# Performance work log

Measured on AMD Instinct MI355X. Metric: run time of the kernel, lower is better.

Reference implementation:

```python
import jax, jax.numpy as jnp
import numpy as np

N_NODES = 50000
N_EDGES = 1600000
N_GRAPHS = 64
D = 128


def setup_inputs() -> dict:
    key = jax.random.key(0)
    ks = jax.random.split(key, 6)
    x = jax.random.normal(ks[0], (N_NODES, D), dtype=jnp.float32)
    W1 = jax.random.normal(ks[1], (D, D), dtype=jnp.float32) * (1.0 / np.sqrt(D))
    b1 = jnp.zeros((D,), dtype=jnp.float32)
    W2 = jax.random.normal(ks[2], (D, D), dtype=jnp.float32) * (1.0 / np.sqrt(D))
    b2 = jnp.zeros((D,), dtype=jnp.float32)
    edge_index = jax.random.randint(ks[3], (2, N_EDGES), 0, N_NODES, dtype=jnp.int64)
    batch = jnp.sort(jax.random.randint(ks[4], (N_NODES,), 0, N_GRAPHS, dtype=jnp.int64))
    return {"x": x, "W1": W1, "b1": b1, "W2": W2, "b2": b2,
            "edge_index": edge_index, "batch": batch}


def _gcn_conv(x, W, b, src, dst, coef, n_nodes):
    # GCNConv: h = W^T x; out_i = sum_{j->i} norm_ij * h_j + b
    h = x @ W                                  # [N, D_out]
    msg = h[src] * coef[:, None]               # [E+N, D_out] gather + scale
    out = jax.ops.segment_sum(msg, dst, num_segments=n_nodes)
    return out + b


def reference(x, W1, b1, W2, b2, edge_index, batch):
    n_nodes = x.shape[0]
    # add self-loops (PyG GCNConv default add_self_loops=True)
    loop = jnp.arange(n_nodes, dtype=edge_index.dtype)
    src = jnp.concatenate([edge_index[0], loop])
    dst = jnp.concatenate([edge_index[1], loop])
    # symmetric normalization: deg counted on target side incl. self-loops
    deg = jax.ops.segment_sum(jnp.ones_like(dst, dtype=x.dtype), dst,
                              num_segments=n_nodes)
    dinv = jnp.where(deg > 0, jax.lax.rsqrt(deg), 0.0)
    coef = dinv[src] * dinv[dst]               # [E+N]

    h = jax.nn.relu(_gcn_conv(x, W1, b1, src, dst, coef, n_nodes))
    h = jax.nn.relu(_gcn_conv(h, W2, b2, src, dst, coef, n_nodes))

    # global_mean_pool over batch ids
    sums = jax.ops.segment_sum(h, batch, num_segments=N_GRAPHS)
    cnts = jax.ops.segment_sum(jnp.ones((n_nodes,), dtype=h.dtype), batch,
                               num_segments=N_GRAPHS)
    return sums / jnp.maximum(cnts, 1.0)[:, None]
```

## Files before the change

### kernel.cpp

```cpp
#include <hip/hip_runtime.h>
#include <stdint.h>

#define DF 128
#define PAD 80
#define BCAP 8192
#define PCHUNK 16

typedef __attribute__((ext_vector_type(8))) __bf16 bf16x8;
typedef __attribute__((ext_vector_type(4))) float f32x4;

__device__ inline unsigned bf16rn(float x) {
    unsigned u = __float_as_uint(x);
    return (u + 0x7FFFu + ((u >> 16) & 1u)) >> 16;
}
__device__ inline float4 unpack_bf16x4(uint2 v) {
    float4 r;
    r.x = __uint_as_float(v.x << 16);
    r.y = __uint_as_float(v.x & 0xFFFF0000u);
    r.z = __uint_as_float(v.y << 16);
    r.w = __uint_as_float(v.y & 0xFFFF0000u);
    return r;
}

__global__ __launch_bounds__(256) void bucket_kernel(const int* __restrict__ src,
        const int* __restrict__ dst, int* __restrict__ gcursor,
        unsigned* __restrict__ buckets, int E) {
    __shared__ int hist[256];
    __shared__ int base[256];
    __shared__ int loc[256];
    int tid = threadIdx.x;
    hist[tid] = 0; loc[tid] = 0;
    __syncthreads();
    int beg = blockIdx.x * BCAP;
    int end = beg + BCAP; if (end > E) end = E;
    for (int i = beg + tid; i < end; i += 256) {
        int d = dst[i];
        atomicAdd(&hist[d >> 8], 1);
    }
    __syncthreads();
    base[tid] = atomicAdd(&gcursor[tid], hist[tid]);
    __syncthreads();
    for (int i = beg + tid; i < end; i += 256) {
        int d = dst[i];
        int s = __builtin_nontemporal_load(src + i);
        int b = d >> 8;
        int r = atomicAdd(&loc[b], 1);
        int pos = base[b] + r;
        if (pos < BCAP)
            buckets[(size_t)b * BCAP + pos] = ((unsigned)(d & 255) << 16) | (unsigned)s;
    }
}

__global__ __launch_bounds__(256) void csr_kernel(const unsigned* __restrict__ buckets,
        const int* __restrict__ gcursor, unsigned short* __restrict__ csr,
        int* __restrict__ cnt, float* __restrict__ dinv, int N) {
    __shared__ int nodecnt[256];
    int tid = threadIdx.x;
    nodecnt[tid] = 0;
    __syncthreads();
    int b = blockIdx.x;
    int nb = gcursor[b]; if (nb > BCAP) nb = BCAP;
    const unsigned* __restrict__ bk = buckets + (size_t)b * BCAP;
    for (int i = tid; i < nb; i += 256) {
        unsigned w = bk[i];
        int dl = w >> 16;
        int r = atomicAdd(&nodecnt[dl], 1);
        if (r < PAD)
            csr[(size_t)(b * 256 + dl) * PAD + r] = (unsigned short)(w & 0xFFFFu);
    }
    __syncthreads();
    int node = b * 256 + tid;
    if (node < N) {
        int c = nodecnt[tid];
        cnt[node] = c;
        dinv[node] = rsqrtf((float)(c + 1));
    }
}

__global__ void bounds_kernel(const int* __restrict__ batch, int* __restrict__ gse, int n, int G) {
    int i = blockIdx.x * blockDim.x + threadIdx.x;
    if (i < n) {
        int b = batch[i];
        if (i == 0 || batch[i - 1] != b) gse[b] = i;
        if (i == n - 1 || batch[i + 1] != b) gse[G + b] = i + 1;
    }
}

__global__ __launch_bounds__(256) void gemm_mfma(
    const float* __restrict__ A, const float* __restrict__ W,
    const float* __restrict__ dinv, uint2* __restrict__ g2, int N)
{
    __shared__ unsigned short Wt[128 * 136];
    int tid = threadIdx.x;
    int wv = tid >> 6;
    int l  = tid & 63;
    int lr = l & 15;
    int lk = (l >> 4) * 8;
    int r  = blockIdx.x * 64 + wv * 16 + lr;
    int rc = (r < N) ? r : (N - 1);

    float4 areg[8];
    const float* Arow = A + (size_t)rc * DF;
    #pragma unroll
    for (int ks = 0; ks < 4; ++ks) {
        areg[2 * ks]     = *(const float4*)(Arow + ks * 32 + lk);
        areg[2 * ks + 1] = *(const float4*)(Arow + ks * 32 + lk + 4);
    }

    #pragma unroll
    for (int i = 0; i < 16; ++i) {
        int flat = i * 256 + tid;
        int k = flat >> 5;
        int c4 = (flat & 31) << 2;
        float4 w4 = *(const float4*)(W + (size_t)k * DF + c4);
        Wt[(c4 + 0) * 136 + k] = (unsigned short)bf16rn(w4.x);
        Wt[(c4 + 1) * 136 + k] = (unsigned short)bf16rn(w4.y);
        Wt[(c4 + 2) * 136 + k] = (unsigned short)bf16rn(w4.z);
        Wt[(c4 + 3) * 136 + k] = (unsigned short)bf16rn(w4.w);
    }

    union U8 { unsigned short s[8]; bf16x8 v; };
    bf16x8 aH[4], aL[4];
    #pragma unroll
    for (int ks = 0; ks < 4; ++ks) {
        U8 uh, ul;
        const float* f0 = (const float*)&areg[2 * ks];
        #pragma unroll
        for (int j = 0; j < 8; ++j) {
            float a = f0[j];
            unsigned hb = bf16rn(a);
            float hf = __uint_as_float(hb << 16);
            uh.s[j] = (unsigned short)hb;
            ul.s[j] = (unsigned short)bf16rn(a - hf);
        }
        aH[ks] = uh.v; aL[ks] = ul.v;
    }

    __syncthreads();

    f32x4 zero = {0.f, 0.f, 0.f, 0.f};
    f32x4 acc[8];
    #pragma unroll
    for (int t = 0; t < 8; ++t) acc[t] = zero;

    #pragma unroll
    for (int ks = 0; ks < 4; ++ks) {
        int ko = ks * 32 + lk;
        #pragma unroll
        for (int t = 0; t < 8; ++t) {
            bf16x8 wf = *(const bf16x8*)&Wt[(t * 16 + lr) * 136 + ko];
            acc[t] = __builtin_amdgcn_mfma_f32_16x16x32_bf16(wf, aH[ks], acc[t], 0, 0, 0);
            acc[t] = __builtin_amdgcn_mfma_f32_16x16x32_bf16(wf, aL[ks], acc[t], 0, 0, 0);
        }
    }

    if (r < N) {
        float di = dinv[r];
        int hi4 = l >> 4;
        #pragma unroll
        for (int t = 0; t < 8; ++t) {
            unsigned lo = bf16rn(di * acc[t][0]) | (bf16rn(di * acc[t][1]) << 16);
            unsigned hi = bf16rn(di * acc[t][2]) | (bf16rn(di * acc[t][3]) << 16);
            uint2 o; o.x = lo; o.y = hi;
            g2[(size_t)r * 32 + t * 4 + hi4] = o;
        }
    }
}

__global__ __launch_bounds__(256) void agg_kernel(
    const uint2* __restrict__ g, const unsigned short* __restrict__ csr,
    const int* __restrict__ cnt, const float* __restrict__ dinv,
    const float* __restrict__ bias, float* __restrict__ out, int n)
{
    int idx = blockIdx.x * 256 + threadIdx.x;
    int node = idx >> 5;
    int lane = threadIdx.x & 31;
    if (node >= n) return;
    int deg = cnt[node]; if (deg > PAD) deg = PAD;
    const unsigned short* __restrict__ row = csr + (size_t)node * PAD;

    float4 a0 = unpack_bf16x4(g[(size_t)node * 32 + lane]);
    float4 a1 = {0.f, 0.f, 0.f, 0.f};
    float4 a2 = {0.f, 0.f, 0.f, 0.f};
    float4 a3 = {0.f, 0.f, 0.f, 0.f};

    int e = 0;
    for (; e + 7 < deg; e += 8) {
        uint4 w = *(const uint4*)(row + e);
        int s0 = (int)(w.x & 0xFFFFu), s1 = (int)(w.x >> 16);
        int s2 = (int)(w.y & 0xFFFFu), s3 = (int)(w.y >> 16);
        int s4 = (int)(w.z & 0xFFFFu), s5 = (int)(w.z >> 16);
        int s6 = (int)(w.w & 0xFFFFu), s7 = (int)(w.w >> 16);
        uint2 v0 = g[(size_t)s0 * 32 + lane];
        uint2 v1 = g[(size_t)s1 * 32 + lane];
        uint2 v2 = g[(size_t)s2 * 32 + lane];
        uint2 v3 = g[(size_t)s3 * 32 + lane];
        uint2 v4 = g[(size_t)s4 * 32 + lane];
        uint2 v5 = g[(size_t)s5 * 32 + lane];
        uint2 v6 = g[(size_t)s6 * 32 + lane];
        uint2 v7 = g[(size_t)s7 * 32 + lane];
        float4 f0 = unpack_bf16x4(v0), f1 = unpack_bf16x4(v1);
        float4 f2 = unpack_bf16x4(v2), f3 = unpack_bf16x4(v3);
        float4 f4 = unpack_bf16x4(v4), f5 = unpack_bf16x4(v5);
        float4 f6 = unpack_bf16x4(v6), f7 = unpack_bf16x4(v7);
        a0.x += f0.x + f4.x; a0.y += f0.y + f4.y; a0.z += f0.z + f4.z; a0.w += f0.w + f4.w;
        a1.x += f1.x + f5.x; a1.y += f1.y + f5.y; a1.z += f1.z + f5.z; a1.w += f1.w + f5.w;
        a2.x += f2.x + f6.x; a2.y += f2.y + f6.y; a2.z += f2.z + f6.z; a2.w += f2.w + f6.w;
        a3.x += f3.x + f7.x; a3.y += f3.y + f7.y; a3.z += f3.z + f7.z; a3.w += f3.w + f7.w;
    }
    for (; e + 3 < deg; e += 4) {
        int s0 = row[e], s1 = row[e + 1], s2 = row[e + 2], s3 = row[e + 3];
        uint2 v0 = g[(size_t)s0 * 32 + lane];
        uint2 v1 = g[(size_t)s1 * 32 + lane];
        uint2 v2 = g[(size_t)s2 * 32 + lane];
        uint2 v3 = g[(size_t)s3 * 32 + lane];
        float4 f0 = unpack_bf16x4(v0), f1 = unpack_bf16x4(v1);
        float4 f2 = unpack_bf16x4(v2), f3 = unpack_bf16x4(v3);
        a0.x += f0.x; a0.y += f0.y; a0.z += f0.z; a0.w += f0.w;
        a1.x += f1.x; a1.y += f1.y; a1.z += f1.z; a1.w += f1.w;
        a2.x += f2.x; a2.y += f2.y; a2.z += f2.z; a2.w += f2.w;
        a3.x += f3.x; a3.y += f3.y; a3.z += f3.z; a3.w += f3.w;
    }
    for (; e < deg; ++e) {
        uint2 v = g[(size_t)row[e] * 32 + lane];
        float4 f = unpack_bf16x4(v);
        a0.x += f.x; a0.y += f.y; a0.z += f.z; a0.w += f.w;
    }
    float sx = (a0.x + a1.x) + (a2.x + a3.x);
    float sy = (a0.y + a1.y) + (a2.y + a3.y);
    float sz = (a0.z + a1.z) + (a2.z + a3.z);
    float sw = (a0.w + a1.w) + (a2.w + a3.w);

    float di = dinv[node];
    float4 b4 = ((const float4*)bias)[lane];
    float4 o;
    o.x = fmaxf(fmaf(di, sx, b4.x), 0.f);
    o.y = fmaxf(fmaf(di, sy, b4.y), 0.f);
    o.z = fmaxf(fmaf(di, sz, b4.z), 0.f);
    o.w = fmaxf(fmaf(di, sw, b4.w), 0.f);
    ((float4*)out)[(size_t)node * 32 + lane] = o;
}

__global__ __launch_bounds__(256) void pool_partial(
    const float* __restrict__ h, const int* __restrict__ gse,
    float* __restrict__ acc, int G)
{
    __shared__ float part[256];
    int gi = blockIdx.x >> 4;
    int ck = blockIdx.x & (PCHUNK - 1);
    int s = gse[gi], e = gse[G + gi];
    int len = e - s;
    if (len <= 0) return;
    int per = (len + PCHUNK - 1) / PCHUNK;
    int r0 = s + ck * per;
    int r1 = r0 + per; if (r1 > e) r1 = e;
    int c = threadIdx.x & 127;
    int rr = threadIdx.x >> 7;
    float sum = 0.f;
    for (int r = r0 + rr; r < r1; r += 2) sum += h[(size_t)r * DF + c];
    part[threadIdx.x] = sum;
    __syncthreads();
    if (threadIdx.x < 128) {
        float t = part[threadIdx.x] + part[threadIdx.x + 128];
        atomicAdd(&acc[gi * DF + c], t);
    }
}

__global__ __launch_bounds__(128) void pool_final(
    const float* __restrict__ acc, const int* __restrict__ gse,
    float* __restrict__ out, int G)
{
    int gi = blockIdx.x;
    int c = threadIdx.x;
    int s = gse[gi], e = gse[G + gi];
    out[gi * DF + c] = (e > s) ? (acc[gi * DF + c] / (float)(e - s)) : 0.f;
}

extern "C" void kernel_launch(void* const* d_in, const int* in_sizes, int n_in,
                              void* d_out, int out_size, void* d_ws, size_t ws_size,
                              hipStream_t stream)
{
    const float* x     = (const float*)d_in[0];
    const float* W1    = (const float*)d_in[1];
    const float* b1    = (const float*)d_in[2];
    const float* W2    = (const float*)d_in[3];
    const float* b2    = (const float*)d_in[4];
    const int*   ei    = (const int*)d_in[5];
    const int*   batch = (const int*)d_in[6];

    int N = in_sizes[0] / DF;
    int E = in_sizes[5] / 2;
    int G = out_size / DF;
    const int* src = ei;
    const int* dst = ei + E;

    int nbuck = (N + 255) >> 8;

    char* p = (char*)d_ws;
    int* gcursor = (int*)p; p += (size_t)256 * 4;
    int* gse     = (int*)p; p += (size_t)2 * G * 4;
    float* acc   = (float*)p; p += (size_t)G * DF * 4;
    int* cnt     = (int*)p; p += (size_t)N * 4;
    float* dinv  = (float*)p; p += (size_t)N * 4;
    unsigned* buckets = (unsigned*)p; p += (size_t)nbuck * BCAP * 4;
    unsigned short* csr = (unsigned short*)p; p += (size_t)N * PAD * 2;
    p = (char*)(((uintptr_t)p + 15) & ~(uintptr_t)15);
    uint2* g2 = (uint2*)p; p += (size_t)N * DF * 2;
    float* h  = (float*)p; p += (size_t)N * DF * 4;

    hipMemsetAsync(gcursor, 0, (size_t)(256 + 2 * G + G * DF) * 4, stream);

    const int thr = 256;
    int nb1 = (E + BCAP - 1) / BCAP;

    bounds_kernel<<<(N + thr - 1) / thr, thr, 0, stream>>>(batch, gse, N, G);
    bucket_kernel<<<nb1, thr, 0, stream>>>(src, dst, gcursor, buckets, E);
    csr_kernel<<<nbuck, thr, 0, stream>>>(buckets, gcursor, csr, cnt, dinv, N);

    int gemm_grid = (N + 63) / 64;
    int agg_grid  = (N * 32 + 255) / 256;

    gemm_mfma<<<gemm_grid, thr, 0, stream>>>(x, W1, dinv, g2, N);
    agg_kernel<<<agg_grid, thr, 0, stream>>>(g2, csr, cnt, dinv, b1, h, N);
    gemm_mfma<<<gemm_grid, thr, 0, stream>>>(h, W2, dinv, g2, N);
    agg_kernel<<<agg_grid, thr, 0, stream>>>(g2, csr, cnt, dinv, b2, h, N);
    pool_partial<<<G * PCHUNK, thr, 0, stream>>>(h, gse, acc, G);
    pool_final<<<G, 128, 0, stream>>>(acc, gse, (float*)d_out, G);
}
```

Before: 216.6 us.

## Fuse mean-pool partial sums into second aggregation and merge bounds into CSR build

The second aggregation kernel now stages each block's 8 output rows in shared memory and accumulates per-graph column sums with atomics, replacing the separate pool_partial kernel that re-read h. The graph-boundary computation moves into csr_kernel, which removes one launch. The gather loop is unrolled to 16 neighbours per iteration to keep more loads in flight. The cost is more atomics (one set per block) plus a __syncthreads and shared memory in the aggregation kernel; the output h is still written even though the pooled path no longer needs it.

Result: no change. 220.1 us (+1.6%).

```diff
diff --git a/kernel.cpp b/kernel.cpp
--- a/kernel.cpp
+++ b/kernel.cpp
@@ -4,7 +4,6 @@
 #define DF 128
 #define PAD 80
 #define BCAP 8192
-#define PCHUNK 16
 
 typedef __attribute__((ext_vector_type(8))) __bf16 bf16x8;
 typedef __attribute__((ext_vector_type(4))) float f32x4;
@@ -20,6 +19,9 @@
     r.z = __uint_as_float(v.y << 16);
     r.w = __uint_as_float(v.y & 0xFFFF0000u);
     return r;
+}
+__device__ inline void addf4(float4& a, float4 f) {
+    a.x += f.x; a.y += f.y; a.z += f.z; a.w += f.w;
 }
 
 __global__ __launch_bounds__(256) void bucket_kernel(const int* __restrict__ src,
@@ -53,7 +55,8 @@
 
 __global__ __launch_bounds__(256) void csr_kernel(const unsigned* __restrict__ buckets,
         const int* __restrict__ gcursor, unsigned short* __restrict__ csr,
-        int* __restrict__ cnt, float* __restrict__ dinv, int N) {
+        int* __restrict__ cnt, float* __restrict__ dinv,
+        const int* __restrict__ batch, int* __restrict__ gse, int N, int G) {
     __shared__ int nodecnt[256];
     int tid = threadIdx.x;
     nodecnt[tid] = 0;
@@ -74,15 +77,9 @@
         int c = nodecnt[tid];
         cnt[node] = c;
         dinv[node] = rsqrtf((float)(c + 1));
-    }
-}
-
-__global__ void bounds_kernel(const int* __restrict__ batch, int* __restrict__ gse, int n, int G) {
-    int i = blockIdx.x * blockDim.x + threadIdx.x;
-    if (i < n) {
-        int b = batch[i];
-        if (i == 0 || batch[i - 1] != b) gse[b] = i;
-        if (i == n - 1 || batch[i + 1] != b) gse[G + b] = i + 1;
+        int bg = batch[node];
+        if (node == 0 || batch[node - 1] != bg) gse[bg] = node;
+        if (node == N - 1 || batch[node + 1] != bg) gse[G + bg] = node + 1;
     }
 }
 
@@ -167,102 +164,106 @@
     }
 }
 
+template<bool POOL>
 __global__ __launch_bounds__(256) void agg_kernel(
     const uint2* __restrict__ g, const unsigned short* __restrict__ csr,
     const int* __restrict__ cnt, const float* __restrict__ dinv,
-    const float* __restrict__ bias, float* __restrict__ out, int n)
+    const float* __restrict__ bias, float* __restrict__ out,
+    const int* __restrict__ batch, float* __restrict__ acc, int n)
 {
+    __shared__ float hrow[8 * 128];
+    __shared__ int gids[8];
     int idx = blockIdx.x * 256 + threadIdx.x;
     int node = idx >> 5;
     int lane = threadIdx.x & 31;
-    if (node >= n) return;
-    int deg = cnt[node]; if (deg > PAD) deg = PAD;
-    const unsigned short* __restrict__ row = csr + (size_t)node * PAD;
-
-    float4 a0 = unpack_bf16x4(g[(size_t)node * 32 + lane]);
-    float4 a1 = {0.f, 0.f, 0.f, 0.f};
-    float4 a2 = {0.f, 0.f, 0.f, 0.f};
-    float4 a3 = {0.f, 0.f, 0.f, 0.f};
-
-    int e = 0;
-    for (; e + 7 < deg; e += 8) {
-        uint4 w = *(const uint4*)(row + e);
-        int s0 = (int)(w.x & 0xFFFFu), s1 = (int)(w.x >> 16);
-        int s2 = (int)(w.y & 0xFFFFu), s3 = (int)(w.y >> 16);
-        int s4 = (int)(w.z & 0xFFFFu), s5 = (int)(w.z >> 16);
-        int s6 = (int)(w.w & 0xFFFFu), s7 = (int)(w.w >> 16);
-        uint2 v0 = g[(size_t)s0 * 32 + lane];
-        uint2 v1 = g[(size_t)s1 * 32 + lane];
-        uint2 v2 = g[(size_t)s2 * 32 + lane];
-        uint2 v3 = g[(size_t)s3 * 32 + lane];
-        uint2 v4 = g[(size_t)s4 * 32 + lane];
-        uint2 v5 = g[(size_t)s5 * 32 + lane];
-        uint2 v6 = g[(size_t)s6 * 32 + lane];
-        uint2 v7 = g[(size_t)s7 * 32 + lane];
-        float4 f0 = unpack_bf16x4(v0), f1 = unpack_bf16x4(v1);
-        float4 f2 = unpack_bf16x4(v2), f3 = unpack_bf16x4(v3);
-        float4 f4 = unpack_bf16x4(v4), f5 = unpack_bf16x4(v5);
-        float4 f6 = unpack_bf16x4(v6), f7 = unpack_bf16x4(v7);
-        a0.x += f0.x + f4.x; a0.y += f0.y + f4.y; a0.z += f0.z + f4.z; a0.w += f0.w + f4.w;
-        a1.x += f1.x + f5.x; a1.y += f1.y + f5.y; a1.z += f1.z + f5.z; a1.w += f1.w + f5.w;
-        a2.x += f2.x + f6.x; a2.y += f2.y + f6.y; a2.z += f2.z + f6.z; a2.w += f2.w + f6.w;
-        a3.x += f3.x + f7.x; a3.y += f3.y + f7.y; a3.z += f3.z + f7.z; a3.w += f3.w + f7.w;
-    }
-    for (; e + 3 < deg; e += 4) {
-        int s0 = row[e], s1 = row[e + 1], s2 = row[e + 2], s3 = row[e + 3];
-        uint2 v0 = g[(size_t)s0 * 32 + lane];
-        uint2 v1 = g[(size_t)s1 * 32 + lane];
-        uint2 v2 = g[(size_t)s2 * 32 + lane];
-        uint2 v3 = g[(size_t)s3 * 32 + lane];
-        float4 f0 = unpack_bf16x4(v0), f1 = unpack_bf16x4(v1);
-        float4 f2 = unpack_bf16x4(v2), f3 = unpack_bf16x4(v3);
-        a0.x += f0.x; a0.y += f0.y; a0.z += f0.z; a0.w += f0.w;
-        a1.x += f1.x; a1.y += f1.y; a1.z += f1.z; a1.w += f1.w;
-        a2.x += f2.x; a2.y += f2.y; a2.z += f2.z; a2.w += f2.w;
-        a3.x += f3.x; a3.y += f3.y; a3.z += f3.z; a3.w += f3.w;
-    }
-    for (; e < deg; ++e) {
-        uint2 v = g[(size_t)row[e] * 32 + lane];
-        float4 f = unpack_bf16x4(v);
-        a0.x += f.x; a0.y += f.y; a0.z += f.z; a0.w += f.w;
-    }
-    float sx = (a0.x + a1.x) + (a2.x + a3.x);
-    float sy = (a0.y + a1.y) + (a2.y + a3.y);
-    float sz = (a0.z + a1.z) + (a2.z + a3.z);
-    float sw = (a0.w + a1.w) + (a2.w + a3.w);
-
-    float di = dinv[node];
-    float4 b4 = ((const float4*)bias)[lane];
-    float4 o;
-    o.x = fmaxf(fmaf(di, sx, b4.x), 0.f);
-    o.y = fmaxf(fmaf(di, sy, b4.y), 0.f);
-    o.z = fmaxf(fmaf(di, sz, b4.z), 0.f);
-    o.w = fmaxf(fmaf(di, sw, b4.w), 0.f);
-    ((float4*)out)[(size_t)node * 32 + lane] = o;
-}
-
-__global__ __launch_bounds__(256) void pool_partial(
-    const float* __restrict__ h, const int* __restrict__ gse,
-    float* __restrict__ acc, int G)
-{
-    __shared__ float part[256];
-    int gi = blockIdx.x >> 4;
-    int ck = blockIdx.x & (PCHUNK - 1);
-    int s = gse[gi], e = gse[G + gi];
-    int len = e - s;
-    if (len <= 0) return;
-    int per = (len + PCHUNK - 1) / PCHUNK;
-    int r0 = s + ck * per;
-    int r1 = r0 + per; if (r1 > e) r1 = e;
-    int c = threadIdx.x & 127;
-    int rr = threadIdx.x >> 7;
-    float sum = 0.f;
-    for (int r = r0 + rr; r < r1; r += 2) sum += h[(size_t)r * DF + c];
-    part[threadIdx.x] = sum;
-    __syncthreads();
-    if (threadIdx.x < 128) {
-        float t = part[threadIdx.x] + part[threadIdx.x + 128];
-        atomicAdd(&acc[gi * DF + c], t);
+    bool active = node < n;
+
+    float4 a0 = {0,0,0,0}, a1 = {0,0,0,0}, a2 = {0,0,0,0}, a3 = {0,0,0,0};
+    float4 o  = {0,0,0,0};
+
+    if (active) {
+        int deg = cnt[node]; if (deg > PAD) deg = PAD;
+        const unsigned short* __restrict__ row = csr + (size_t)node * PAD;
+        a0 = unpack_bf16x4(g[(size_t)node * 32 + lane]);
+
+        int e = 0;
+        for (; e + 15 < deg; e += 16) {
+            uint4 wA = *(const uint4*)(row + e);
+            uint4 wB = *(const uint4*)(row + e + 8);
+            uint2 v0 = g[(size_t)(wA.x & 0xFFFFu) * 32 + lane];
+            uint2 v1 = g[(size_t)(wA.x >> 16)     * 32 + lane];
+            uint2 v2 = g[(size_t)(wA.y & 0xFFFFu) * 32 + lane];
+            uint2 v3 = g[(size_t)(wA.y >> 16)     * 32 + lane];
+            uint2 v4 = g[(size_t)(wA.z & 0xFFFFu) * 32 + lane];
+            uint2 v5 = g[(size_t)(wA.z >> 16)     * 32 + lane];
+            uint2 v6 = g[(size_t)(wA.w & 0xFFFFu) * 32 + lane];
+            uint2 v7 = g[(size_t)(wA.w >> 16)     * 32 + lane];
+            uint2 u0 = g[(size_t)(wB.x & 0xFFFFu) * 32 + lane];
+            uint2 u1 = g[(size_t)(wB.x >> 16)     * 32 + lane];
+            uint2 u2 = g[(size_t)(wB.y & 0xFFFFu) * 32 + lane];
+            uint2 u3 = g[(size_t)(wB.y >> 16)     * 32 + lane];
+            uint2 u4 = g[(size_t)(wB.z & 0xFFFFu) * 32 + lane];
+            uint2 u5 = g[(size_t)(wB.z >> 16)     * 32 + lane];
+            uint2 u6 = g[(size_t)(wB.w & 0xFFFFu) * 32 + lane];
+            uint2 u7 = g[(size_t)(wB.w >> 16)     * 32 + lane];
+            addf4(a0, unpack_bf16x4(v0)); addf4(a1, unpack_bf16x4(v1));
+            addf4(a2, unpack_bf16x4(v2)); addf4(a3, unpack_bf16x4(v3));
+            addf4(a0, unpack_bf16x4(v4)); addf4(a1, unpack_bf16x4(v5));
+            addf4(a2, unpack_bf16x4(v6)); addf4(a3, unpack_bf16x4(v7));
+            addf4(a0, unpack_bf16x4(u0)); addf4(a1, unpack_bf16x4(u1));
+            addf4(a2, unpack_bf16x4(u2)); addf4(a3, unpack_bf16x4(u3));
+            addf4(a0, unpack_bf16x4(u4)); addf4(a1, unpack_bf16x4(u5));
+            addf4(a2, unpack_bf16x4(u6)); addf4(a3, unpack_bf16x4(u7));
+        }
+        for (; e + 3 < deg; e += 4) {
+            int s0 = row[e], s1 = row[e + 1], s2 = row[e + 2], s3 = row[e + 3];
+            uint2 v0 = g[(size_t)s0 * 32 + lane];
+            uint2 v1 = g[(size_t)s1 * 32 + lane];
+            uint2 v2 = g[(size_t)s2 * 32 + lane];
+            uint2 v3 = g[(size_t)s3 * 32 + lane];
+            addf4(a0, unpack_bf16x4(v0)); addf4(a1, unpack_bf16x4(v1));
+            addf4(a2, unpack_bf16x4(v2)); addf4(a3, unpack_bf16x4(v3));
+        }
+        for (; e < deg; ++e) {
+            uint2 v = g[(size_t)row[e] * 32 + lane];
+            addf4(a0, unpack_bf16x4(v));
+        }
+        float sx = (a0.x + a1.x) + (a2.x + a3.x);
+        float sy = (a0.y + a1.y) + (a2.y + a3.y);
+        float sz = (a0.z + a1.z) + (a2.z + a3.z);
+        float sw = (a0.w + a1.w) + (a2.w + a3.w);
+
+        float di = dinv[node];
+        float4 b4 = ((const float4*)bias)[lane];
+        o.x = fmaxf(fmaf(di, sx, b4.x), 0.f);
+        o.y = fmaxf(fmaf(di, sy, b4.y), 0.f);
+        o.z = fmaxf(fmaf(di, sz, b4.z), 0.f);
+        o.w = fmaxf(fmaf(di, sw, b4.w), 0.f);
+        ((float4*)out)[(size_t)node * 32 + lane] = o;
+    }
+
+    if (POOL) {
+        int lnode = threadIdx.x >> 5;
+        float* hr = hrow + lnode * 128 + lane * 4;
+        hr[0] = o.x; hr[1] = o.y; hr[2] = o.z; hr[3] = o.w;
+        if (lane == 0) gids[lnode] = active ? batch[node] : -1;
+        __syncthreads();
+        if (threadIdx.x < 128) {
+            int c = threadIdx.x;
+            int prev = gids[0];
+            float s = 0.f;
+            #pragma unroll
+            for (int rr = 0; rr < 8; ++rr) {
+                int gd = gids[rr];
+                if (gd < 0) break;
+                if (gd != prev) {
+                    if (prev >= 0) atomicAdd(&acc[prev * 128 + c], s);
+                    s = 0.f; prev = gd;
+                }
+                s += hrow[rr * 128 + c];
+            }
+            if (prev >= 0) atomicAdd(&acc[prev * 128 + c], s);
+        }
     }
 }
 
@@ -313,17 +314,15 @@
     const int thr = 256;
     int nb1 = (E + BCAP - 1) / BCAP;
 
-    bounds_kernel<<<(N + thr - 1) / thr, thr, 0, stream>>>(batch, gse, N, G);
     bucket_kernel<<<nb1, thr, 0, stream>>>(src, dst, gcursor, buckets, E);
-    csr_kernel<<<nbuck, thr, 0, stream>>>(buckets, gcursor, csr, cnt, dinv, N);
+    csr_kernel<<<nbuck, thr, 0, stream>>>(buckets, gcursor, csr, cnt, dinv, batch, gse, N, G);
 
     int gemm_grid = (N + 63) / 64;
     int agg_grid  = (N * 32 + 255) / 256;
 
     gemm_mfma<<<gemm_grid, thr, 0, stream>>>(x, W1, dinv, g2, N);
-    agg_kernel<<<agg_grid, thr, 0, stream>>>(g2, csr, cnt, dinv, b1, h, N);
+    agg_kernel<false><<<agg_grid, thr, 0, stream>>>(g2, csr, cnt, dinv, b1, h, batch, acc, N);
     gemm_mfma<<<gemm_grid, thr, 0, stream>>>(h, W2, dinv, g2, N);
-    agg_kernel<<<agg_grid, thr, 0, stream>>>(g2, csr, cnt, dinv, b2, h, N);
-    pool_partial<<<G * PCHUNK, thr, 0, stream>>>(h, gse, acc, G);
+    agg_kernel<true><<<agg_grid, thr, 0, stream>>>(g2, csr, cnt, dinv, b2, h, batch, acc, N);
     pool_final<<<G, 128, 0, stream>>>(acc, gse, (float*)d_out, G);
 }
```

## Replace global-atomic bucketing with per-chunk bucket cells and fuse graph bounds

Applied to the files above, without the earlier changes.

The edge bucketing step drops its histogram pass and global atomic cursor. Each chunk block now writes its edges into a private fixed-capacity cell for each destination bucket and records a per-chunk count. The CSR kernel walks those cells serially per thread, and the batch-boundary computation is folded into it, removing one launch and one read pass over dst. The risk is that serial per-thread cell scans can be slower than the old coalesced bucket reads, and cells capped at CCAP silently drop overflow edges.

New measurement: 239.8 us. 1.11x slower.

```diff
diff --git a/kernel.cpp b/kernel.cpp
--- a/kernel.cpp
+++ b/kernel.cpp
@@ -4,6 +4,7 @@
 #define DF 128
 #define PAD 80
 #define BCAP 8192
+#define CCAP 96
 #define PCHUNK 16
 
 typedef __attribute__((ext_vector_type(8))) __bf16 bf16x8;
@@ -21,52 +22,58 @@
     r.w = __uint_as_float(v.y & 0xFFFF0000u);
     return r;
 }
-
-__global__ __launch_bounds__(256) void bucket_kernel(const int* __restrict__ src,
-        const int* __restrict__ dst, int* __restrict__ gcursor,
-        unsigned* __restrict__ buckets, int E) {
-    __shared__ int hist[256];
-    __shared__ int base[256];
+__device__ inline void addf4(float4& a, float4 f) {
+    a.x += f.x; a.y += f.y; a.z += f.z; a.w += f.w;
+}
+
+__global__ __launch_bounds__(256) void bucket_sp(const int* __restrict__ src,
+        const int* __restrict__ dst, unsigned* __restrict__ buckets,
+        int* __restrict__ cnts, int E, int nchunk, int nbuck) {
     __shared__ int loc[256];
     int tid = threadIdx.x;
-    hist[tid] = 0; loc[tid] = 0;
-    __syncthreads();
-    int beg = blockIdx.x * BCAP;
+    loc[tid] = 0;
+    __syncthreads();
+    int chunk = blockIdx.x;
+    int beg = chunk * BCAP;
     int end = beg + BCAP; if (end > E) end = E;
     for (int i = beg + tid; i < end; i += 256) {
         int d = dst[i];
-        atomicAdd(&hist[d >> 8], 1);
-    }
-    __syncthreads();
-    base[tid] = atomicAdd(&gcursor[tid], hist[tid]);
-    __syncthreads();
-    for (int i = beg + tid; i < end; i += 256) {
-        int d = dst[i];
-        int s = __builtin_nontemporal_load(src + i);
+        int s = src[i];
         int b = d >> 8;
-        int r = atomicAdd(&loc[b], 1);
-        int pos = base[b] + r;
-        if (pos < BCAP)
-            buckets[(size_t)b * BCAP + pos] = ((unsigned)(d & 255) << 16) | (unsigned)s;
-    }
-}
-
-__global__ __launch_bounds__(256) void csr_kernel(const unsigned* __restrict__ buckets,
-        const int* __restrict__ gcursor, unsigned short* __restrict__ csr,
-        int* __restrict__ cnt, float* __restrict__ dinv, int N) {
+        int slot = atomicAdd(&loc[b], 1);
+        if (slot < CCAP)
+            buckets[((size_t)b * nchunk + chunk) * CCAP + slot] =
+                ((unsigned)(d & 255) << 16) | (unsigned)s;
+    }
+    __syncthreads();
+    for (int b = tid; b < nbuck; b += 256) {
+        int c = loc[b]; if (c > CCAP) c = CCAP;
+        cnts[(size_t)b * nchunk + chunk] = c;
+    }
+}
+
+__global__ __launch_bounds__(256) void csr_sp(const unsigned* __restrict__ buckets,
+        const int* __restrict__ cnts, unsigned short* __restrict__ csr,
+        int* __restrict__ cnt, float* __restrict__ dinv,
+        const int* __restrict__ batch, int* __restrict__ gse,
+        int N, int G, int nchunk) {
     __shared__ int nodecnt[256];
     int tid = threadIdx.x;
     nodecnt[tid] = 0;
     __syncthreads();
     int b = blockIdx.x;
-    int nb = gcursor[b]; if (nb > BCAP) nb = BCAP;
-    const unsigned* __restrict__ bk = buckets + (size_t)b * BCAP;
-    for (int i = tid; i < nb; i += 256) {
-        unsigned w = bk[i];
-        int dl = w >> 16;
-        int r = atomicAdd(&nodecnt[dl], 1);
-        if (r < PAD)
-            csr[(size_t)(b * 256 + dl) * PAD + r] = (unsigned short)(w & 0xFFFFu);
+    const unsigned* __restrict__ bk = buckets + (size_t)b * nchunk * CCAP;
+    const int* __restrict__ cr = cnts + (size_t)b * nchunk;
+    for (int c = tid; c < nchunk; c += 256) {
+        int nb = cr[c];
+        const unsigned* __restrict__ cell = bk + (size_t)c * CCAP;
+        for (int i = 0; i < nb; ++i) {
+            unsigned w = cell[i];
+            int dl = w >> 16;
+            int r = atomicAdd(&nodecnt[dl], 1);
+            if (r < PAD)
+                csr[(size_t)(b * 256 + dl) * PAD + r] = (unsigned short)(w & 0xFFFFu);
+        }
     }
     __syncthreads();
     int node = b * 256 + tid;
@@ -74,15 +81,9 @@
         int c = nodecnt[tid];
         cnt[node] = c;
         dinv[node] = rsqrtf((float)(c + 1));
-    }
-}
-
-__global__ void bounds_kernel(const int* __restrict__ batch, int* __restrict__ gse, int n, int G) {
-    int i = blockIdx.x * blockDim.x + threadIdx.x;
-    if (i < n) {
-        int b = batch[i];
-        if (i == 0 || batch[i - 1] != b) gse[b] = i;
-        if (i == n - 1 || batch[i + 1] != b) gse[G + b] = i + 1;
+        int bg = batch[node];
+        if (node == 0 || batch[node - 1] != bg) gse[bg] = node;
+        if (node == N - 1 || batch[node + 1] != bg) gse[G + bg] = node + 1;
     }
 }
 
@@ -199,14 +200,10 @@
         uint2 v5 = g[(size_t)s5 * 32 + lane];
         uint2 v6 = g[(size_t)s6 * 32 + lane];
         uint2 v7 = g[(size_t)s7 * 32 + lane];
-        float4 f0 = unpack_bf16x4(v0), f1 = unpack_bf16x4(v1);
-        float4 f2 = unpack_bf16x4(v2), f3 = unpack_bf16x4(v3);
-        float4 f4 = unpack_bf16x4(v4), f5 = unpack_bf16x4(v5);
-        float4 f6 = unpack_bf16x4(v6), f7 = unpack_bf16x4(v7);
-        a0.x += f0.x + f4.x; a0.y += f0.y + f4.y; a0.z += f0.z + f4.z; a0.w += f0.w + f4.w;
-        a1.x += f1.x + f5.x; a1.y += f1.y + f5.y; a1.z += f1.z + f5.z; a1.w += f1.w + f5.w;
-        a2.x += f2.x + f6.x; a2.y += f2.y + f6.y; a2.z += f2.z + f6.z; a2.w += f2.w + f6.w;
-        a3.x += f3.x + f7.x; a3.y += f3.y + f7.y; a3.z += f3.z + f7.z; a3.w += f3.w + f7.w;
+        addf4(a0, unpack_bf16x4(v0)); addf4(a1, unpack_bf16x4(v1));
+        addf4(a2, unpack_bf16x4(v2)); addf4(a3, unpack_bf16x4(v3));
+        addf4(a0, unpack_bf16x4(v4)); addf4(a1, unpack_bf16x4(v5));
+        addf4(a2, unpack_bf16x4(v6)); addf4(a3, unpack_bf16x4(v7));
     }
     for (; e + 3 < deg; e += 4) {
         int s0 = row[e], s1 = row[e + 1], s2 = row[e + 2], s3 = row[e + 3];
@@ -214,17 +211,12 @@
         uint2 v1 = g[(size_t)s1 * 32 + lane];
         uint2 v2 = g[(size_t)s2 * 32 + lane];
         uint2 v3 = g[(size_t)s3 * 32 + lane];
-        float4 f0 = unpack_bf16x4(v0), f1 = unpack_bf16x4(v1);
-        float4 f2 = unpack_bf16x4(v2), f3 = unpack_bf16x4(v3);
-        a0.x += f0.x; a0.y += f0.y; a0.z += f0.z; a0.w += f0.w;
-        a1.x += f1.x; a1.y += f1.y; a1.z += f1.z; a1.w += f1.w;
-        a2.x += f2.x; a2.y += f2.y; a2.z += f2.z; a2.w += f2.w;
-        a3.x += f3.x; a3.y += f3.y; a3.z += f3.z; a3.w += f3.w;
+        addf4(a0, unpack_bf16x4(v0)); addf4(a1, unpack_bf16x4(v1));
+        addf4(a2, unpack_bf16x4(v2)); addf4(a3, unpack_bf16x4(v3));
     }
     for (; e < deg; ++e) {
         uint2 v = g[(size_t)row[e] * 32 + lane];
-        float4 f = unpack_bf16x4(v);
-        a0.x += f.x; a0.y += f.y; a0.z += f.z; a0.w += f.w;
+        addf4(a0, unpack_bf16x4(v));
     }
     float sx = (a0.x + a1.x) + (a2.x + a3.x);
     float sy = (a0.y + a1.y) + (a2.y + a3.y);
@@ -294,28 +286,27 @@
     const int* src = ei;
     const int* dst = ei + E;
 
-    int nbuck = (N + 255) >> 8;
+    int nbuck  = (N + 255) >> 8;
+    int nchunk = (E + BCAP - 1) / BCAP;
 
     char* p = (char*)d_ws;
-    int* gcursor = (int*)p; p += (size_t)256 * 4;
     int* gse     = (int*)p; p += (size_t)2 * G * 4;
     float* acc   = (float*)p; p += (size_t)G * DF * 4;
     int* cnt     = (int*)p; p += (size_t)N * 4;
     float* dinv  = (float*)p; p += (size_t)N * 4;
-    unsigned* buckets = (unsigned*)p; p += (size_t)nbuck * BCAP * 4;
+    int* cnts    = (int*)p; p += (size_t)nbuck * nchunk * 4;
+    unsigned* buckets = (unsigned*)p; p += (size_t)nbuck * nchunk * CCAP * 4;
     unsigned short* csr = (unsigned short*)p; p += (size_t)N * PAD * 2;
     p = (char*)(((uintptr_t)p + 15) & ~(uintptr_t)15);
     uint2* g2 = (uint2*)p; p += (size_t)N * DF * 2;
     float* h  = (float*)p; p += (size_t)N * DF * 4;
 
-    hipMemsetAsync(gcursor, 0, (size_t)(256 + 2 * G + G * DF) * 4, stream);
+    hipMemsetAsync(gse, 0, (size_t)(2 * G + G * DF) * 4, stream);
 
     const int thr = 256;
-    int nb1 = (E + BCAP - 1) / BCAP;
-
-    bounds_kernel<<<(N + thr - 1) / thr, thr, 0, stream>>>(batch, gse, N, G);
-    bucket_kernel<<<nb1, thr, 0, stream>>>(src, dst, gcursor, buckets, E);
-    csr_kernel<<<nbuck, thr, 0, stream>>>(buckets, gcursor, csr, cnt, dinv, N);
+
+    bucket_sp<<<nchunk, thr, 0, stream>>>(src, dst, buckets, cnts, E, nchunk, nbuck);
+    csr_sp<<<nbuck, thr, 0, stream>>>(buckets, cnts, csr, cnt, dinv, batch, gse, N, G, nchunk);
 
     int gemm_grid = (N + 63) / 64;
     int agg_grid  = (N * 32 + 255) / 256;
```
